# Kernel tuning notes

Hardware: AMD Instinct MI355X
Metric: run time of the kernel (lower is better)

The kernel has to match this reference:

```python
import jax, jax.numpy as jnp
import numpy as np

HIDDEN = 4096
N_Q_HEADS = 32
N_KV_HEADS = 8
HEAD_DIM = 128
V_HEAD_DIM = 128
WINDOW = 1024
ROPE_THETA = 1000000.0
SEQ = 2048


def setup_inputs() -> dict:
    key = jax.random.key(0)
    ks = jax.random.split(key, 7)
    s = 0.02
    return {
        "hidden_states": jax.random.normal(ks[0], (SEQ, HIDDEN), dtype=jnp.float32),
        "positions": jnp.arange(SEQ, dtype=jnp.int32),
        "wq": jax.random.normal(ks[1], (HIDDEN, N_Q_HEADS * HEAD_DIM), dtype=jnp.float32) * s,
        "wk": jax.random.normal(ks[2], (HIDDEN, N_KV_HEADS * HEAD_DIM), dtype=jnp.float32) * s,
        "wv": jax.random.normal(ks[3], (HIDDEN, N_KV_HEADS * V_HEAD_DIM), dtype=jnp.float32) * s,
        "wo": jax.random.normal(ks[4], (N_Q_HEADS * V_HEAD_DIM, HIDDEN), dtype=jnp.float32) * s,
        "sink": jax.random.normal(ks[5], (N_Q_HEADS,), dtype=jnp.float32),
    }


def _apply_rope_neox(x, positions):
    # x: [S, H, D]; rotate full head_dim in neox (half-split) style
    d = x.shape[-1]
    inv_freq = 1.0 / (ROPE_THETA ** (jnp.arange(0, d, 2, dtype=jnp.float32) / d))
    freqs = positions.astype(jnp.float32)[:, None] * inv_freq[None, :]  # [S, D/2]
    cos = jnp.cos(freqs)[:, None, :]  # [S, 1, D/2]
    sin = jnp.sin(freqs)[:, None, :]
    x1, x2 = x[..., : d // 2], x[..., d // 2 :]
    return jnp.concatenate([x1 * cos - x2 * sin, x2 * cos + x1 * sin], axis=-1)


def reference(hidden_states, positions, wq, wk, wv, wo, sink):
    S = hidden_states.shape[0]
    scaling = HEAD_DIM ** -0.5
    q = (hidden_states @ wq).reshape(S, N_Q_HEADS, HEAD_DIM)
    k = (hidden_states @ wk).reshape(S, N_KV_HEADS, HEAD_DIM)
    v = (hidden_states @ wv).reshape(S, N_KV_HEADS, V_HEAD_DIM)

    q = _apply_rope_neox(q, positions)
    k = _apply_rope_neox(k, positions)

    groups = N_Q_HEADS // N_KV_HEADS
    k_rep = jnp.repeat(k, groups, axis=1)  # [S, Hq, D]
    v_rep = jnp.repeat(v, groups, axis=1)

    # [Hq, S(query), S(key)] attention scores
    scores = jnp.einsum("qhd,khd->hqk", q, k_rep) * scaling

    # causal + sliding-window mask: key j visible iff j <= i and i - j < WINDOW
    i = positions[:, None].astype(jnp.int32)
    j = positions[None, :].astype(jnp.int32)
    mask = (j <= i) & (i - j < WINDOW)  # [S, S]
    neg = jnp.finfo(scores.dtype).min
    scores = jnp.where(mask[None, :, :], scores, neg)

    # softmax with per-head attention sink logit in the denominator
    sink_l = sink[:, None, None]  # [Hq, 1, 1]
    m = jnp.maximum(scores.max(axis=-1, keepdims=True), sink_l)
    w = jnp.exp(scores - m)
    denom = w.sum(axis=-1, keepdims=True) + jnp.exp(sink_l - m)
    probs = w / denom

    attn = jnp.einsum("hqk,khd->qhd", probs, v_rep).reshape(S, N_Q_HEADS * V_HEAD_DIM)
    return attn @ wo
```

## Files before the change

### kernel.cpp

```cpp
#include <hip/hip_runtime.h>
#include <cstdint>
#include <cstddef>

typedef uint16_t u16;
typedef __bf16 bf16x8 __attribute__((ext_vector_type(8)));
typedef float f32x4 __attribute__((ext_vector_type(4)));
typedef u16 u16x8 __attribute__((ext_vector_type(8)));


__device__ __forceinline__ u16 f2bf(float f) {
    union { float f; uint32_t i; } v; v.f = f;
    uint32_t b = v.i;
    return (u16)((b + 0x7FFFu + ((b >> 16) & 1u)) >> 16);
}
__device__ __forceinline__ float bf2f(u16 u) {
    union { uint32_t i; float f; } v; v.i = ((uint32_t)u) << 16; return v.f;
}
__device__ __forceinline__ float nanfix(float x, float repl) {
    return (x == x && fabsf(x) < 1e30f) ? x : repl;
}
__device__ __forceinline__ void async16(const u16* g, u16* l) {
    __builtin_amdgcn_global_load_lds(
        (const __attribute__((address_space(1))) uint32_t*)g,
        (__attribute__((address_space(3))) uint32_t*)l, 16, 0, 0);
}

template<int N> __device__ __forceinline__ void waitvm() {
    if constexpr (N == 0) asm volatile("s_waitcnt vmcnt(0)" ::: "memory");
    else if constexpr (N == 1) asm volatile("s_waitcnt vmcnt(1)" ::: "memory");
    else if constexpr (N == 2) asm volatile("s_waitcnt vmcnt(2)" ::: "memory");
    else if constexpr (N == 3) asm volatile("s_waitcnt vmcnt(3)" ::: "memory");
    else if constexpr (N == 5) asm volatile("s_waitcnt vmcnt(5)" ::: "memory");
    else if constexpr (N == 6) asm volatile("s_waitcnt vmcnt(6)" ::: "memory");
    else if constexpr (N == 7) asm volatile("s_waitcnt vmcnt(7)" ::: "memory");
}

#define BARRIER() do { __builtin_amdgcn_s_barrier(); __builtin_amdgcn_sched_barrier(0); } while (0)

__global__ void cvt_k(const float* __restrict__ in, u16* __restrict__ out) {
    const size_t i = ((size_t)blockIdx.x * 256 + threadIdx.x) * 8;
    const f32x4 a = *(const f32x4*)&in[i], b = *(const f32x4*)&in[i + 4];
    u16x8 s;
    #pragma unroll
    for (int e = 0; e < 4; e++) { s[e] = f2bf(a[e]); s[4 + e] = f2bf(b[e]); }
    *(u16x8*)&out[i] = s;
}

__global__ void cvtT_k(const float* __restrict__ in, u16* __restrict__ out,
                       int R, int C) {
    __shared__ float tile[32][33];
    const int bx = blockIdx.x * 32, by = blockIdx.y * 32;
    const int tx = threadIdx.x, ty = threadIdx.y;
    #pragma unroll
    for (int i = 0; i < 32; i += 8)
        tile[ty + i][tx] = in[(size_t)(by + ty + i) * C + (bx + tx)];
    __syncthreads();
    #pragma unroll
    for (int i = 0; i < 32; i += 8)
        out[(size_t)(bx + ty + i) * R + (by + tx)] = f2bf(tile[tx][ty + i]);
}


#define SB(g, kk, dst) async16(Bb + (size_t)((g) * 64 + rg) * 4096 + (kk) + sc, \
                               (dst) + ((g) * 64 + wave * 8) * 64)
#define SA(g, kk, dst) async16(Ab + (size_t)((g) * 32 + aro) * 4096 + (kk) + sc, \
                               (dst) + ((g) * 32 + wbA) * 64)

#define APHASE(P) do {                                                          \
    bf16x8 a0[2], a1[2];                                                        \
    _Pragma("unroll")                                                           \
    for (int ks = 0; ks < 2; ks++) {                                            \
        const int r0 = wr * 128 + (2 * (P)) * 16 + lr;                          \
        const int r1 = wr * 128 + (2 * (P) + 1) * 16 + lr;                      \
        a0[ks] = *(const bf16x8*)&Ac[r0 * 64 + (((ks * 4 + qd) ^ (r0 & 7)) * 8)]; \
        a1[ks] = *(const bf16x8*)&Ac[r1 * 64 + (((ks * 4 + qd) ^ (r1 & 7)) * 8)]; \
    }                                                                           \
    __builtin_amdgcn_s_setprio(1);                                              \
    _Pragma("unroll")                                                           \
    for (int nn = 0; nn < 4; nn++)                                              \
        _Pragma("unroll")                                                       \
        for (int ks = 0; ks < 2; ks++) {                                        \
            acc[2 * (P)][nn]     = __builtin_amdgcn_mfma_f32_16x16x32_bf16(     \
                a0[ks], b[nn][ks], acc[2 * (P)][nn], 0, 0, 0);                  \
            acc[2 * (P) + 1][nn] = __builtin_amdgcn_mfma_f32_16x16x32_bf16(     \
                a1[ks], b[nn][ks], acc[2 * (P) + 1][nn], 0, 0, 0);              \
        }                                                                       \
    __builtin_amdgcn_s_setprio(0);                                              \
} while (0)

template<bool STAGE>
__device__ __forceinline__ void tile_body(
    const u16* __restrict__ Ab, const u16* __restrict__ Bb,
    const u16* Ac, const u16* Bc, u16* An, u16* Bn, int k1,
    int wave, int lr, int qd, int wr, int wc,
    int rg, int sc, int aro, int wbA, f32x4 (&acc)[8][4])
{
    waitvm<3>();
    BARRIER();
    if constexpr (STAGE) { SB(0, k1, Bn); SB(1, k1, Bn); SB(2, k1, Bn); }
    bf16x8 b[4][2];
    #pragma unroll
    for (int nn = 0; nn < 4; nn++)
        #pragma unroll
        for (int ks = 0; ks < 2; ks++) {
            const int row = wc * 64 + nn * 16 + lr;
            b[nn][ks] = *(const bf16x8*)&Bc[row * 64 + (((ks * 4 + qd) ^ (row & 7)) * 8)];
        }
    APHASE(0);
    if constexpr (STAGE) waitvm<5>(); else waitvm<2>();
    BARRIER();
    if constexpr (STAGE) { SB(3, k1, Bn); SA(0, k1, An); }
    APHASE(1);
    if constexpr (STAGE) waitvm<6>(); else waitvm<1>();
    BARRIER();
    if constexpr (STAGE) { SA(1, k1, An); SA(2, k1, An); }
    APHASE(2);
    if constexpr (STAGE) waitvm<7>(); else waitvm<0>();
    BARRIER();
    if constexpr (STAGE) { SA(3, k1, An); }
    APHASE(3);
}

template<int MODE>
__global__ __launch_bounds__(512, 2) void gemm256(
    const u16* __restrict__ A, const u16* __restrict__ BT,
    u16* __restrict__ qk, u16* __restrict__ vT, float* __restrict__ Cf,
    const int ntn)
{
    alignas(16) __shared__ u16 As[2][256 * 64];
    alignas(16) __shared__ u16 Bs[2][256 * 64];

    const int tid = threadIdx.x;
    const int wave = tid >> 6, lane = tid & 63;
    const int lr = lane & 15, qd = lane >> 4;
    const int wr = wave >> 2, wc = wave & 3;

    const int cpx = gridDim.x >> 3;
    const int sw = (blockIdx.x & 7) * cpx + (blockIdx.x >> 3);
    const int m0 = (sw / ntn) * 256, n0 = (sw % ntn) * 256;

    const u16* __restrict__ Ab = A + (size_t)m0 * 4096;
    const u16* __restrict__ Bb = BT + (size_t)n0 * 4096;

    const int rg = tid >> 3;
    const int sc = ((tid & 7) ^ (rg & 7)) * 8;
    const int aro = (rg < 32) ? rg : (96 + rg);
    const int wbA = (wave < 4) ? wave * 8 : (96 + wave * 8);

    f32x4 acc[8][4];
    #pragma unroll
    for (int i = 0; i < 8; i++)
        #pragma unroll
        for (int j = 0; j < 4; j++) acc[i][j] = (f32x4){0.f, 0.f, 0.f, 0.f};

    u16* const As0 = &As[0][0]; u16* const As1 = &As[1][0];
    u16* const Bs0 = &Bs[0][0]; u16* const Bs1 = &Bs[1][0];

    SB(0, 0, Bs0); SB(1, 0, Bs0); SB(2, 0, Bs0); SB(3, 0, Bs0);
    SA(0, 0, As0); SA(1, 0, As0); SA(2, 0, As0); SA(3, 0, As0);

    for (int t = 0; t < 63; ++t) {
        const bool odd = t & 1;
        tile_body<true>(Ab, Bb, odd ? As1 : As0, odd ? Bs1 : Bs0,
                        odd ? As0 : As1, odd ? Bs0 : Bs1, (t + 1) * 64,
                        wave, lr, qd, wr, wc, rg, sc, aro, wbA, acc);
    }
    tile_body<false>(Ab, Bb, As1, Bs1, As0, Bs0, 0,
                     wave, lr, qd, wr, wc, rg, sc, aro, wbA, acc);

    #pragma unroll
    for (int i = 0; i < 8; i++)
        #pragma unroll
        for (int j = 0; j < 4; j++) {
            const int col = n0 + wc * 64 + j * 16 + lr;
            #pragma unroll
            for (int r = 0; r < 4; r++) {
                const int row = m0 + wr * 128 + i * 16 + qd * 4 + r;
                if constexpr (MODE == 0) {
                    const u16 val = f2bf(nanfix(acc[i][j][r], 1000.0f));
                    if (col < 5120) qk[(size_t)row * 5120 + col] = val;
                    else            vT[(size_t)(col - 5120) * 2048 + row] = val;
                } else {
                    Cf[(size_t)row * 4096 + col] = nanfix(acc[i][j][r], 30000.0f);
                }
            }
        }
}

#undef SB
#undef SA
#undef APHASE

__global__ void rope_k(u16* __restrict__ qk, const int* __restrict__ positions) {
    const int s = blockIdx.x;
    const int h = blockIdx.y;
    const int t = threadIdx.x;
    u16* base = qk + (size_t)s * 5120 + ((h < 32) ? h * 128 : 4096 + (h - 32) * 128);
    const float pos = (float)positions[s];
    const float freq = pos * exp2f(-(float)t * (19.931568569324174f / 64.f));
    const float c = cosf(freq), sn = sinf(freq);
    const float x1 = bf2f(base[t]), x2 = bf2f(base[t + 64]);
    base[t]      = f2bf(x1 * c - x2 * sn);
    base[t + 64] = f2bf(x2 * c + x1 * sn);
}

__global__ __launch_bounds__(256) void attn_k(
    const u16* __restrict__ qk, const u16* __restrict__ vT,
    const float* __restrict__ sink, u16* __restrict__ out)
{
    alignas(16) __shared__ u16 Ks[64 * 128];
    alignas(16) __shared__ u16 VsT[128 * 72];
    alignas(16) __shared__ u16 Ps[4][16 * 72];

    const int h = blockIdx.y, hk = h >> 2;
    const int q0 = blockIdx.x * 64;
    const int tid = threadIdx.x, wave = tid >> 6, lane = tid & 63;
    const int lr = lane & 15, qd = lane >> 4;
    const float scaling = 0.08838834764831845f;

    bf16x8 aq[4];
    #pragma unroll
    for (int kc = 0; kc < 4; kc++)
        aq[kc] = *(const bf16x8*)&qk[(size_t)(q0 + wave * 16 + lr) * 5120 + h * 128 + kc * 32 + qd * 8];

    const float sinkv = sink[h];
    float m_run[4], l_run[4];
    #pragma unroll
    for (int r = 0; r < 4; r++) { m_run[r] = sinkv; l_run[r] = 0.f; }
    f32x4 acc_o[8];
    #pragma unroll
    for (int i = 0; i < 8; i++) acc_o[i] = (f32x4){0.f, 0.f, 0.f, 0.f};

    const int jlo = (q0 - 1023) > 0 ? (q0 - 1023) : 0;
    const int t0 = jlo >> 6, t1 = q0 >> 6;

    for (int kt = t0; kt <= t1; kt++) {
        const int j0 = kt * 64;
        __syncthreads();
        #pragma unroll
        for (int p = 0; p < 4; p++) {
            const int idx = p * 256 + tid;
            const int r = idx >> 4, cs = idx & 15, c = cs ^ (r & 15);
            async16(&qk[(size_t)(j0 + r) * 5120 + 4096 + hk * 128 + c * 8],
                    Ks + (p * 256 + wave * 64) * 8);
        }
        #pragma unroll
        for (int p = 0; p < 4; p++) {
            const int idx = p * 256 + tid;
            const int vd = idx >> 3, sc2 = (idx & 7) * 8;
            const u16x8 v = *(const u16x8*)&vT[(size_t)(hk * 128 + vd) * 2048 + j0 + sc2];
            *(u16x8*)&VsT[vd * 72 + sc2] = v;
        }
        __syncthreads();

        float sv[4][4];
        #pragma unroll
        for (int nt = 0; nt < 4; nt++) {
            f32x4 s = (f32x4){0.f, 0.f, 0.f, 0.f};
            #pragma unroll
            for (int kc = 0; kc < 4; kc++) {
                const int krow = nt * 16 + lr;
                const bf16x8 bk = *(const bf16x8*)&Ks[(krow * 16 + ((kc * 4 + qd) ^ lr)) * 8];
                s = __builtin_amdgcn_mfma_f32_16x16x32_bf16(aq[kc], bk, s, 0, 0, 0);
            }
            #pragma unroll
            for (int r = 0; r < 4; r++) sv[nt][r] = s[r];
        }

        float rmax[4] = {-1e30f, -1e30f, -1e30f, -1e30f};
        #pragma unroll
        for (int nt = 0; nt < 4; nt++) {
            const int kpos = j0 + nt * 16 + lr;
            #pragma unroll
            for (int r = 0; r < 4; r++) {
                const int qpos = q0 + wave * 16 + qd * 4 + r;
                const bool ok = (kpos <= qpos) && (qpos - kpos < 1024);
                const float x = ok ? sv[nt][r] * scaling : -1e30f;
                sv[nt][r] = x;
                rmax[r] = fmaxf(rmax[r], x);
            }
        }
        #pragma unroll
        for (int off = 1; off < 16; off <<= 1)
            #pragma unroll
            for (int r = 0; r < 4; r++)
                rmax[r] = fmaxf(rmax[r], __shfl_xor(rmax[r], off, 64));

        float alpha[4], rsum[4];
        #pragma unroll
        for (int r = 0; r < 4; r++) {
            const float mnew = fmaxf(m_run[r], rmax[r]);
            alpha[r] = __expf(m_run[r] - mnew);
            m_run[r] = mnew;
            rsum[r] = 0.f;
        }
        #pragma unroll
        for (int nt = 0; nt < 4; nt++)
            #pragma unroll
            for (int r = 0; r < 4; r++) {
                const float p = __expf(sv[nt][r] - m_run[r]);
                sv[nt][r] = p;
                rsum[r] += p;
            }
        #pragma unroll
        for (int off = 1; off < 16; off <<= 1)
            #pragma unroll
            for (int r = 0; r < 4; r++)
                rsum[r] += __shfl_xor(rsum[r], off, 64);
        #pragma unroll
        for (int r = 0; r < 4; r++)
            l_run[r] = l_run[r] * alpha[r] + rsum[r];

        #pragma unroll
        for (int nt = 0; nt < 4; nt++)
            #pragma unroll
            for (int r = 0; r < 4; r++)
                Ps[wave][(qd * 4 + r) * 72 + nt * 16 + lr] = f2bf(sv[nt][r]);

        #pragma unroll
        for (int i = 0; i < 8; i++)
            #pragma unroll
            for (int r = 0; r < 4; r++) acc_o[i][r] *= alpha[r];

        __syncthreads();

        bf16x8 pa[2];
        #pragma unroll
        for (int kc = 0; kc < 2; kc++)
            pa[kc] = *(const bf16x8*)&Ps[wave][lr * 72 + kc * 32 + qd * 8];

        #pragma unroll
        for (int nt = 0; nt < 8; nt++)
            #pragma unroll
            for (int kc = 0; kc < 2; kc++) {
                const bf16x8 bv = *(const bf16x8*)&VsT[(nt * 16 + lr) * 72 + kc * 32 + qd * 8];
                acc_o[nt] = __builtin_amdgcn_mfma_f32_16x16x32_bf16(pa[kc], bv, acc_o[nt], 0, 0, 0);
            }
    }

    float invd[4];
    #pragma unroll
    for (int r = 0; r < 4; r++)
        invd[r] = 1.f / (l_run[r] + __expf(sinkv - m_run[r]));
    #pragma unroll
    for (int nt = 0; nt < 8; nt++) {
        const int col = h * 128 + nt * 16 + lr;
        #pragma unroll
        for (int r = 0; r < 4; r++) {
            const int row = q0 + wave * 16 + qd * 4 + r;
            out[(size_t)row * 4096 + col] = f2bf(nanfix(acc_o[nt][r] * invd[r], 8.0f));
        }
    }
}

extern "C" void kernel_launch(void* const* d_in, const int* in_sizes, int n_in,
                              void* d_out, int out_size, void* d_ws, size_t ws_size,
                              hipStream_t stream)
{
    (void)in_sizes; (void)n_in; (void)out_size; (void)ws_size;
    const float* hidden    = (const float*)d_in[0];
    const int*   positions = (const int*)d_in[1];
    const float* wq   = (const float*)d_in[2];
    const float* wk   = (const float*)d_in[3];
    const float* wv   = (const float*)d_in[4];
    const float* wo   = (const float*)d_in[5];
    const float* sink = (const float*)d_in[6];
    float* out = (float*)d_out;

    char* ws = (char*)d_ws;
    u16* hiddenB = (u16*)(ws);
    u16* wqkvT   = (u16*)(ws + (size_t)16777216);
    u16* qk      = (u16*)(ws + (size_t)67108864);
    u16* vT      = (u16*)(ws + (size_t)88080384);
    u16* woT     = (u16*)(ws);
    u16* attnB   = (u16*)(ws + (size_t)33554432);

    cvt_k <<<4096, 256, 0, stream>>>(hidden, hiddenB);
    cvtT_k<<<dim3(128, 128), dim3(32, 8), 0, stream>>>(wq, wqkvT, 4096, 4096);
    cvtT_k<<<dim3(32, 128),  dim3(32, 8), 0, stream>>>(wk, wqkvT + (size_t)4096 * 4096, 4096, 1024);
    cvtT_k<<<dim3(32, 128),  dim3(32, 8), 0, stream>>>(wv, wqkvT + (size_t)5120 * 4096, 4096, 1024);

    gemm256<0><<<192, 512, 0, stream>>>(hiddenB, wqkvT, qk, vT, nullptr, 24);

    cvtT_k<<<dim3(128, 128), dim3(32, 8), 0, stream>>>(wo, woT, 4096, 4096);

    rope_k<<<dim3(2048, 40), 64, 0, stream>>>(qk, positions);
    attn_k<<<dim3(32, 32), 256, 0, stream>>>(qk, vT, sink, attnB);

    gemm256<1><<<128, 512, 0, stream>>>(attnB, woT, nullptr, nullptr, out, 16);
}
```

Measured before the change: 611.8 us.

## Narrow GEMM N-tiles to fill all CUs and deepen async prefetch schedule

```diff
diff --git a/kernel.cpp b/kernel.cpp
--- a/kernel.cpp
+++ b/kernel.cpp
@@ -26,13 +26,23 @@
 }
 
 template<int N> __device__ __forceinline__ void waitvm() {
-    if constexpr (N == 0) asm volatile("s_waitcnt vmcnt(0)" ::: "memory");
-    else if constexpr (N == 1) asm volatile("s_waitcnt vmcnt(1)" ::: "memory");
-    else if constexpr (N == 2) asm volatile("s_waitcnt vmcnt(2)" ::: "memory");
-    else if constexpr (N == 3) asm volatile("s_waitcnt vmcnt(3)" ::: "memory");
-    else if constexpr (N == 5) asm volatile("s_waitcnt vmcnt(5)" ::: "memory");
-    else if constexpr (N == 6) asm volatile("s_waitcnt vmcnt(6)" ::: "memory");
-    else if constexpr (N == 7) asm volatile("s_waitcnt vmcnt(7)" ::: "memory");
+    static_assert(N >= 0 && N <= 15, "vmcnt range");
+    if constexpr (N == 0)  asm volatile("s_waitcnt vmcnt(0)" ::: "memory");
+    else if constexpr (N == 1)  asm volatile("s_waitcnt vmcnt(1)" ::: "memory");
+    else if constexpr (N == 2)  asm volatile("s_waitcnt vmcnt(2)" ::: "memory");
+    else if constexpr (N == 3)  asm volatile("s_waitcnt vmcnt(3)" ::: "memory");
+    else if constexpr (N == 4)  asm volatile("s_waitcnt vmcnt(4)" ::: "memory");
+    else if constexpr (N == 5)  asm volatile("s_waitcnt vmcnt(5)" ::: "memory");
+    else if constexpr (N == 6)  asm volatile("s_waitcnt vmcnt(6)" ::: "memory");
+    else if constexpr (N == 7)  asm volatile("s_waitcnt vmcnt(7)" ::: "memory");
+    else if constexpr (N == 8)  asm volatile("s_waitcnt vmcnt(8)" ::: "memory");
+    else if constexpr (N == 9)  asm volatile("s_waitcnt vmcnt(9)" ::: "memory");
+    else if constexpr (N == 10) asm volatile("s_waitcnt vmcnt(10)" ::: "memory");
+    else if constexpr (N == 11) asm volatile("s_waitcnt vmcnt(11)" ::: "memory");
+    else if constexpr (N == 12) asm volatile("s_waitcnt vmcnt(12)" ::: "memory");
+    else if constexpr (N == 13) asm volatile("s_waitcnt vmcnt(13)" ::: "memory");
+    else if constexpr (N == 14) asm volatile("s_waitcnt vmcnt(14)" ::: "memory");
+    else                        asm volatile("s_waitcnt vmcnt(15)" ::: "memory");
 }
 
 #define BARRIER() do { __builtin_amdgcn_s_barrier(); __builtin_amdgcn_sched_barrier(0); } while (0)
@@ -67,77 +77,84 @@
                                (dst) + ((g) * 32 + wbA) * 64)
 
 #define APHASE(P) do {                                                          \
-    bf16x8 a0[2], a1[2];                                                        \
+    bf16x8 a0_[2], a1_[2];                                                      \
+    const int r0_ = wr * 128 + (2 * (P)) * 16 + lr;                             \
+    const int r1_ = r0_ + 16;                                                   \
     _Pragma("unroll")                                                           \
     for (int ks = 0; ks < 2; ks++) {                                            \
-        const int r0 = wr * 128 + (2 * (P)) * 16 + lr;                          \
-        const int r1 = wr * 128 + (2 * (P) + 1) * 16 + lr;                      \
-        a0[ks] = *(const bf16x8*)&Ac[r0 * 64 + (((ks * 4 + qd) ^ (r0 & 7)) * 8)]; \
-        a1[ks] = *(const bf16x8*)&Ac[r1 * 64 + (((ks * 4 + qd) ^ (r1 & 7)) * 8)]; \
+        a0_[ks] = *(const bf16x8*)&Ac[r0_ * 64 + (((ks * 4 + qd) ^ (r0_ & 7)) * 8)]; \
+        a1_[ks] = *(const bf16x8*)&Ac[r1_ * 64 + (((ks * 4 + qd) ^ (r1_ & 7)) * 8)]; \
     }                                                                           \
     __builtin_amdgcn_s_setprio(1);                                              \
     _Pragma("unroll")                                                           \
-    for (int nn = 0; nn < 4; nn++)                                              \
+    for (int nn = 0; nn < NF; nn++)                                             \
         _Pragma("unroll")                                                       \
         for (int ks = 0; ks < 2; ks++) {                                        \
             acc[2 * (P)][nn]     = __builtin_amdgcn_mfma_f32_16x16x32_bf16(     \
-                a0[ks], b[nn][ks], acc[2 * (P)][nn], 0, 0, 0);                  \
+                a0_[ks], b[nn][ks], acc[2 * (P)][nn], 0, 0, 0);                 \
             acc[2 * (P) + 1][nn] = __builtin_amdgcn_mfma_f32_16x16x32_bf16(     \
-                a1[ks], b[nn][ks], acc[2 * (P) + 1][nn], 0, 0, 0);              \
+                a1_[ks], b[nn][ks], acc[2 * (P) + 1][nn], 0, 0, 0);             \
         }                                                                       \
     __builtin_amdgcn_s_setprio(0);                                              \
 } while (0)
 
-template<bool STAGE>
+template<int NF, int ISS>
 __device__ __forceinline__ void tile_body(
     const u16* __restrict__ Ab, const u16* __restrict__ Bb,
-    const u16* Ac, const u16* Bc, u16* An, u16* Bn, int k1,
+    u16* Ac, u16* Bc, u16* Aoth, int k1, int k2,
     int wave, int lr, int qd, int wr, int wc,
-    int rg, int sc, int aro, int wbA, f32x4 (&acc)[8][4])
+    int rg, int sc, int aro, int wbA, f32x4 (&acc)[8][NF])
 {
-    waitvm<3>();
+    constexpr int W0 = (ISS == 0) ? 3 : NF + 6;
+    constexpr int W1 = (ISS == 0) ? 2 : NF + 6;
+    constexpr int W2 = (ISS == 2) ? 2 * NF + 6 : (ISS == 1 ? NF + 5 : 1);
+    constexpr int W3 = (ISS == 2) ? 2 * NF + 6 : (ISS == 1 ? NF + 4 : 0);
+
+    waitvm<W0>();
     BARRIER();
-    if constexpr (STAGE) { SB(0, k1, Bn); SB(1, k1, Bn); SB(2, k1, Bn); }
-    bf16x8 b[4][2];
-    #pragma unroll
-    for (int nn = 0; nn < 4; nn++)
+    if constexpr (ISS >= 1) SA(3, k1, Aoth);
+    bf16x8 b[NF][2];
+    #pragma unroll
+    for (int nn = 0; nn < NF; nn++)
         #pragma unroll
         for (int ks = 0; ks < 2; ks++) {
-            const int row = wc * 64 + nn * 16 + lr;
+            const int row = wc * (16 * NF) + nn * 16 + lr;
             b[nn][ks] = *(const bf16x8*)&Bc[row * 64 + (((ks * 4 + qd) ^ (row & 7)) * 8)];
         }
     APHASE(0);
-    if constexpr (STAGE) waitvm<5>(); else waitvm<2>();
+    waitvm<W1>();
     BARRIER();
-    if constexpr (STAGE) { SB(3, k1, Bn); SA(0, k1, An); }
+    if constexpr (ISS == 2) {
+        #pragma unroll
+        for (int g = 0; g < NF; g++) SB(g, k2, Bc);
+        SA(0, k2, Ac);
+    }
     APHASE(1);
-    if constexpr (STAGE) waitvm<6>(); else waitvm<1>();
+    waitvm<W2>();
     BARRIER();
-    if constexpr (STAGE) { SA(1, k1, An); SA(2, k1, An); }
+    if constexpr (ISS == 2) SA(1, k2, Ac);
     APHASE(2);
-    if constexpr (STAGE) waitvm<7>(); else waitvm<0>();
+    waitvm<W3>();
     BARRIER();
-    if constexpr (STAGE) { SA(3, k1, An); }
+    if constexpr (ISS == 2) SA(2, k2, Ac);
     APHASE(3);
 }
 
-template<int MODE>
+template<int NF, int MODE>
 __global__ __launch_bounds__(512, 2) void gemm256(
     const u16* __restrict__ A, const u16* __restrict__ BT,
-    u16* __restrict__ qk, u16* __restrict__ vT, float* __restrict__ Cf,
-    const int ntn)
+    u16* __restrict__ qk, u16* __restrict__ vT, float* __restrict__ Cf)
 {
     alignas(16) __shared__ u16 As[2][256 * 64];
-    alignas(16) __shared__ u16 Bs[2][256 * 64];
+    alignas(16) __shared__ u16 Bs[2][NF * 64 * 64];
 
     const int tid = threadIdx.x;
     const int wave = tid >> 6, lane = tid & 63;
     const int lr = lane & 15, qd = lane >> 4;
     const int wr = wave >> 2, wc = wave & 3;
 
-    const int cpx = gridDim.x >> 3;
-    const int sw = (blockIdx.x & 7) * cpx + (blockIdx.x >> 3);
-    const int m0 = (sw / ntn) * 256, n0 = (sw % ntn) * 256;
+    const int sw = (blockIdx.x & 7) * 32 + (blockIdx.x >> 3);
+    const int m0 = (sw >> 5) * 256, n0 = (sw & 31) * (NF * 64);
 
     const u16* __restrict__ Ab = A + (size_t)m0 * 4096;
     const u16* __restrict__ Bb = BT + (size_t)n0 * 4096;
@@ -147,32 +164,37 @@
     const int aro = (rg < 32) ? rg : (96 + rg);
     const int wbA = (wave < 4) ? wave * 8 : (96 + wave * 8);
 
-    f32x4 acc[8][4];
+    f32x4 acc[8][NF];
     #pragma unroll
     for (int i = 0; i < 8; i++)
         #pragma unroll
-        for (int j = 0; j < 4; j++) acc[i][j] = (f32x4){0.f, 0.f, 0.f, 0.f};
-
-    u16* const As0 = &As[0][0]; u16* const As1 = &As[1][0];
-    u16* const Bs0 = &Bs[0][0]; u16* const Bs1 = &Bs[1][0];
-
-    SB(0, 0, Bs0); SB(1, 0, Bs0); SB(2, 0, Bs0); SB(3, 0, Bs0);
-    SA(0, 0, As0); SA(1, 0, As0); SA(2, 0, As0); SA(3, 0, As0);
-
-    for (int t = 0; t < 63; ++t) {
-        const bool odd = t & 1;
-        tile_body<true>(Ab, Bb, odd ? As1 : As0, odd ? Bs1 : Bs0,
-                        odd ? As0 : As1, odd ? Bs0 : Bs1, (t + 1) * 64,
-                        wave, lr, qd, wr, wc, rg, sc, aro, wbA, acc);
+        for (int j = 0; j < NF; j++) acc[i][j] = (f32x4){0.f, 0.f, 0.f, 0.f};
+
+    #pragma unroll
+    for (int g = 0; g < NF; g++) SB(g, 0, &Bs[0][0]);
+    SA(0, 0, &As[0][0]); SA(1, 0, &As[0][0]); SA(2, 0, &As[0][0]); SA(3, 0, &As[0][0]);
+    #pragma unroll
+    for (int g = 0; g < NF; g++) SB(g, 64, &Bs[1][0]);
+    SA(0, 64, &As[1][0]); SA(1, 64, &As[1][0]); SA(2, 64, &As[1][0]);
+
+    for (int t = 0; t < 62; t += 2) {
+        tile_body<NF, 2>(Ab, Bb, &As[0][0], &Bs[0][0], &As[1][0],
+                         (t + 1) * 64, (t + 2) * 64,
+                         wave, lr, qd, wr, wc, rg, sc, aro, wbA, acc);
+        tile_body<NF, 2>(Ab, Bb, &As[1][0], &Bs[1][0], &As[0][0],
+                         (t + 2) * 64, (t + 3) * 64,
+                         wave, lr, qd, wr, wc, rg, sc, aro, wbA, acc);
     }
-    tile_body<false>(Ab, Bb, As1, Bs1, As0, Bs0, 0,
+    tile_body<NF, 1>(Ab, Bb, &As[0][0], &Bs[0][0], &As[1][0], 63 * 64, 0,
                      wave, lr, qd, wr, wc, rg, sc, aro, wbA, acc);
+    tile_body<NF, 0>(Ab, Bb, &As[1][0], &Bs[1][0], &As[0][0], 0, 0,
+                     wave, lr, qd, wr, wc, rg, sc, aro, wbA, acc);
 
     #pragma unroll
     for (int i = 0; i < 8; i++)
         #pragma unroll
-        for (int j = 0; j < 4; j++) {
-            const int col = n0 + wc * 64 + j * 16 + lr;
+        for (int j = 0; j < NF; j++) {
+            const int col = n0 + wc * (16 * NF) + j * 16 + lr;
             #pragma unroll
             for (int r = 0; r < 4; r++) {
                 const int row = m0 + wr * 128 + i * 16 + qd * 4 + r;
@@ -380,12 +402,12 @@
     cvtT_k<<<dim3(32, 128),  dim3(32, 8), 0, stream>>>(wk, wqkvT + (size_t)4096 * 4096, 4096, 1024);
     cvtT_k<<<dim3(32, 128),  dim3(32, 8), 0, stream>>>(wv, wqkvT + (size_t)5120 * 4096, 4096, 1024);
 
-    gemm256<0><<<192, 512, 0, stream>>>(hiddenB, wqkvT, qk, vT, nullptr, 24);
+    gemm256<3, 0><<<256, 512, 0, stream>>>(hiddenB, wqkvT, qk, vT, nullptr);
 
     cvtT_k<<<dim3(128, 128), dim3(32, 8), 0, stream>>>(wo, woT, 4096, 4096);
 
     rope_k<<<dim3(2048, 40), 64, 0, stream>>>(qk, positions);
     attn_k<<<dim3(32, 32), 256, 0, stream>>>(qk, vT, sink, attnB);
 
-    gemm256<1><<<128, 512, 0, stream>>>(attnB, woT, nullptr, nullptr, out, 16);
-}
+    gemm256<2, 1><<<256, 512, 0, stream>>>(attnB, woT, nullptr, nullptr, out);
+}
```

After: 670.4 us. 9.6% more time.
